# Performance work log

Measured on AMD Instinct MI355X. Metric: run time of the kernel, lower is better.

The kernel has to match this reference:

```python
import jax, jax.numpy as jnp
import numpy as np

B, D = 4096, 2048

def setup_inputs() -> dict:
    key = jax.random.key(0)
    k1, k2 = jax.random.split(key)
    return {
        "cond_feature": jax.random.normal(k1, (B, D), dtype=jnp.float32),
        "sol_feature": jax.random.normal(k2, (B, D), dtype=jnp.float32),
        "temperature": jnp.zeros((), dtype=jnp.float32),
    }

def _l2norm(x):
    # matches torch F.normalize(dim=-1): x / max(||x||, eps)
    n = jnp.linalg.norm(x, axis=-1, keepdims=True)
    return x / jnp.maximum(n, 1e-12)

def reference(cond_feature, sol_feature, temperature):
    c = _l2norm(cond_feature.reshape(cond_feature.shape[0], -1))
    s = _l2norm(sol_feature.reshape(sol_feature.shape[0], -1))
    sim = jnp.einsum('bd,nd->bn', c, s)          # [B, B]
    sim = jnp.maximum(sim, 0.0) * jnp.exp(temperature)
    # cross-entropy with labels = arange(B): mean(logsumexp(row) - diag)
    diag = jnp.diagonal(sim)
    loss_r = jnp.mean(jax.scipy.special.logsumexp(sim, axis=1) - diag)
    loss_c = jnp.mean(jax.scipy.special.logsumexp(sim, axis=0) - diag)
    return (loss_r + loss_c) * 0.5
```

## Files before the change

kernel.cpp:

```cpp
#include <hip/hip_runtime.h>
#include <hip/hip_bf16.h>

#define B_N 4096
#define D_K 2048
#define RB  1024

typedef __attribute__((ext_vector_type(4))) int   i32x4;
typedef __attribute__((ext_vector_type(8))) int   i32x8;
typedef __attribute__((ext_vector_type(4))) float f32x4;

__device__ __forceinline__ i32x8 mk8(i32x4 lo) {
    return (i32x8){lo[0], lo[1], lo[2], lo[3], 0, 0, 0, 0};
}

__device__ __forceinline__ void gl_lds16(const void* g, void* l) {
    __builtin_amdgcn_global_load_lds(
        (const __attribute__((address_space(1))) unsigned int*)g,
        (__attribute__((address_space(3))) unsigned int*)l,
        16, 0, 0);
}

__device__ __forceinline__ unsigned int qe2m1(float v) {
    unsigned int s = (__builtin_bit_cast(unsigned int, v) >> 31) << 3;
    float av = fabsf(v);
    unsigned int c = (av >= 0.25f) + (av >= 0.75f) + (av >= 1.25f) + (av >= 1.75f)
                   + (av >= 2.5f)  + (av >= 3.5f)  + (av >= 5.0f);
    return s | c;
}

__global__ __launch_bounds__(256) void knorm4(const float* __restrict__ C,
                                              const float* __restrict__ S,
                                              unsigned char* __restrict__ Cq,
                                              unsigned char* __restrict__ Sq,
                                              float* __restrict__ rowsum,
                                              float* __restrict__ colsum) {
    int b = blockIdx.x;
    const float* X;
    unsigned char* Y;
    if (b < B_N) { X = C + (size_t)b * D_K; Y = Cq + (size_t)b * RB; }
    else         { X = S + (size_t)(b - B_N) * D_K; Y = Sq + (size_t)(b - B_N) * RB; }
    int tid = threadIdx.x;

    if (tid == 0) {
        if (b < B_N) rowsum[b] = 0.f;
        else         colsum[b - B_N] = 0.f;
    }

    float4 v0 = ((const float4*)X)[tid * 2];
    float4 v1 = ((const float4*)X)[tid * 2 + 1];
    float ss = v0.x*v0.x + v0.y*v0.y + v0.z*v0.z + v0.w*v0.w
             + v1.x*v1.x + v1.y*v1.y + v1.z*v1.z + v1.w*v1.w;
    #pragma unroll
    for (int off = 1; off < 64; off <<= 1) ss += __shfl_xor(ss, off, 64);
    __shared__ float wsum[4];
    if ((tid & 63) == 0) wsum[tid >> 6] = ss;
    __syncthreads();
    float tot = wsum[0] + wsum[1] + wsum[2] + wsum[3];
    float inv = 64.f / fmaxf(sqrtf(tot), 1e-12f);

    float vals[8] = { v0.x, v0.y, v0.z, v0.w, v1.x, v1.y, v1.z, v1.w };
    unsigned int u = 0;
    #pragma unroll
    for (int j = 0; j < 8; ++j)
        u |= qe2m1(vals[j] * inv) << (4 * j);
    *(unsigned int*)(Y + tid * 4) = u;
}


#define SBK 256
#define NST (D_K / SBK)

__global__ __launch_bounds__(256, 2) void kgemm_q4(const unsigned char* __restrict__ Aq,
                                                   const unsigned char* __restrict__ Bq,
                                                   const float* __restrict__ temp,
                                                   float* __restrict__ rowsum,
                                                   float* __restrict__ colsum,
                                                   float* __restrict__ diag) {
    __shared__ __align__(16) unsigned char As[128 * 128];
    __shared__ __align__(16) unsigned char Bs[256 * 128];

    const int tid  = threadIdx.x;
    const int lane = tid & 63;
    const int wn   = tid >> 6;
    const int brow = blockIdx.x * 128;
    const int bcol = blockIdx.y * 256;

    const int srow = tid >> 3;
    const int sch  = ((tid & 7) ^ (srow & 7)) * 16;
    const unsigned char* gA = Aq + (size_t)(brow + srow) * RB + sch;
    const unsigned char* gB = Bq + (size_t)(bcol + srow) * RB + sch;

    const int lrow = lane & 15;
    const int kq   = lane >> 4;
    const int sw   = lrow & 7;
    const int ch0  = ((kq)     ^ sw) * 16;
    const int ch1  = ((4 + kq) ^ sw) * 16;
    const int abase = lrow * 128;
    const int bbase = (wn * 64 + lrow) * 128;

    f32x4 acc[8][4];
    #pragma unroll
    for (int m = 0; m < 8; ++m)
        #pragma unroll
        for (int n = 0; n < 4; ++n) acc[m][n] = (f32x4){0.f, 0.f, 0.f, 0.f};

    for (int st = 0; st < NST; ++st) {
        const int k0b = st * 128;
        #pragma unroll
        for (int i = 0; i < 4; ++i)
            gl_lds16(gA + k0b + (size_t)(32 * i) * RB, As + tid * 16 + i * 4096);
        #pragma unroll
        for (int i = 0; i < 8; ++i)
            gl_lds16(gB + k0b + (size_t)(32 * i) * RB, Bs + tid * 16 + i * 4096);
        __syncthreads();

        #pragma unroll
        for (int h = 0; h < 2; ++h) {
            const int ch = h ? ch1 : ch0;
            i32x4 b0 = *(const i32x4*)(Bs + bbase + 0 * 2048 + ch);
            i32x4 b1 = *(const i32x4*)(Bs + bbase + 1 * 2048 + ch);
            i32x4 b2 = *(const i32x4*)(Bs + bbase + 2 * 2048 + ch);
            i32x4 b3 = *(const i32x4*)(Bs + bbase + 3 * 2048 + ch);
            __builtin_amdgcn_sched_barrier(0);

            #define QMMA(mm) do { \
                i32x4 a_ = *(const i32x4*)(As + abase + (mm) * 2048 + ch); \
                i32x8 a8 = mk8(a_); \
                acc[mm][0] = __builtin_amdgcn_mfma_scale_f32_16x16x128_f8f6f4( \
                    a8, mk8(b0), acc[mm][0], 4, 4, 0, 127, 0, 127); \
                acc[mm][1] = __builtin_amdgcn_mfma_scale_f32_16x16x128_f8f6f4( \
                    a8, mk8(b1), acc[mm][1], 4, 4, 0, 127, 0, 127); \
                acc[mm][2] = __builtin_amdgcn_mfma_scale_f32_16x16x128_f8f6f4( \
                    a8, mk8(b2), acc[mm][2], 4, 4, 0, 127, 0, 127); \
                acc[mm][3] = __builtin_amdgcn_mfma_scale_f32_16x16x128_f8f6f4( \
                    a8, mk8(b3), acc[mm][3], 4, 4, 0, 127, 0, 127); \
                __builtin_amdgcn_sched_barrier(0); \
            } while (0)

            QMMA(0); QMMA(1); QMMA(2); QMMA(3);
            QMMA(4); QMMA(5); QMMA(6); QMMA(7);
            #undef QMMA
        }
        __syncthreads();
    }

    const float scl = expf(temp[0]);
    const int cbase = bcol + wn * 64 + lrow;
    const int rj = kq * 4;

    float cs[4] = {0.f, 0.f, 0.f, 0.f};
    #pragma unroll
    for (int m = 0; m < 8; ++m) {
        float rs[4] = {0.f, 0.f, 0.f, 0.f};
        #pragma unroll
        for (int n = 0; n < 4; ++n) {
            #pragma unroll
            for (int j = 0; j < 4; ++j) {
                float sim = acc[m][n][j] * (1.f / 4096.f);
                float v = fmaxf(sim, 0.f) * scl;
                int gr = brow + m * 16 + rj + j;
                int gc = cbase + n * 16;
                if (gr == gc) diag[gr] = v;
                float p = expf(v - scl);
                rs[j]  += p;
                cs[n]  += p;
            }
        }
        #pragma unroll
        for (int j = 0; j < 4; ++j) {
            float v = rs[j];
            v += __shfl_xor(v, 1, 64);
            v += __shfl_xor(v, 2, 64);
            v += __shfl_xor(v, 4, 64);
            v += __shfl_xor(v, 8, 64);
            if (lrow == 0) atomicAdd(&rowsum[brow + m * 16 + rj + j], v);
        }
    }
    #pragma unroll
    for (int n = 0; n < 4; ++n) {
        float v = cs[n];
        v += __shfl_xor(v, 16, 64);
        v += __shfl_xor(v, 32, 64);
        if (kq == 0) atomicAdd(&colsum[cbase + n * 16], v);
    }
}

__global__ __launch_bounds__(256) void kfinal(const float* __restrict__ rowsum,
                                              const float* __restrict__ colsum,
                                              const float* __restrict__ diag,
                                              const float* __restrict__ temp,
                                              float* __restrict__ out) {
    int tid = threadIdx.x;
    float M = expf(temp[0]);
    float acc = 0.f;
    for (int i = tid; i < B_N; i += 256) {
        acc += logf(rowsum[i]) + logf(colsum[i]) + 2.f * M - 2.f * diag[i];
    }
    #pragma unroll
    for (int off = 1; off < 64; off <<= 1) acc += __shfl_xor(acc, off, 64);
    __shared__ float wsum[4];
    if ((tid & 63) == 0) wsum[tid >> 6] = acc;
    __syncthreads();
    if (tid == 0) {
        float t = wsum[0] + wsum[1] + wsum[2] + wsum[3];
        out[0] = t * (0.5f / (float)B_N);
    }
}

extern "C" void kernel_launch(void* const* d_in, const int* in_sizes, int n_in,
                              void* d_out, int out_size, void* d_ws, size_t ws_size,
                              hipStream_t stream) {
    const float* Cf   = (const float*)d_in[0];
    const float* Sf   = (const float*)d_in[1];
    const float* temp = (const float*)d_in[2];

    const size_t MATB = (size_t)B_N * RB;
    unsigned char* Cq = (unsigned char*)d_ws;
    unsigned char* Sq = Cq + MATB;
    float* rowsum = (float*)(Sq + MATB);
    float* colsum = rowsum + B_N;
    float* diag   = colsum + B_N;

    knorm4<<<2 * B_N, 256, 0, stream>>>(Cf, Sf, Cq, Sq, rowsum, colsum);
    dim3 grid(B_N / 128, B_N / 256);
    kgemm_q4<<<grid, 256, 0, stream>>>(Cq, Sq, temp, rowsum, colsum, diag);
    kfinal<<<1, 256, 0, stream>>>(rowsum, colsum, diag, temp, (float*)d_out);
}
```

Before: 54.61 us.

## Shrink GEMM block tile to 128x128 with 2x2 wave grid

Changes the FP4 GEMM block tile from 128x256 to 128x128 and arranges the four waves as a 2x2 grid, each computing a 64x64 sub-tile instead of 128x64. This halves LDS use and accumulator registers per wave, so more blocks can be resident and the grid has twice as many blocks, which helps fill the GPU. In exchange, more A/B data is reloaded across blocks, and more atomics are issued for the row and column sums.

```diff
diff --git a/kernel.cpp b/kernel.cpp
--- a/kernel.cpp
+++ b/kernel.cpp
@@ -77,13 +77,15 @@
                                                    float* __restrict__ colsum,
                                                    float* __restrict__ diag) {
     __shared__ __align__(16) unsigned char As[128 * 128];
-    __shared__ __align__(16) unsigned char Bs[256 * 128];
+    __shared__ __align__(16) unsigned char Bs[128 * 128];
 
     const int tid  = threadIdx.x;
     const int lane = tid & 63;
-    const int wn   = tid >> 6;
+    const int wid  = tid >> 6;
+    const int wr   = wid >> 1;
+    const int wc   = wid & 1;
     const int brow = blockIdx.x * 128;
-    const int bcol = blockIdx.y * 256;
+    const int bcol = blockIdx.y * 128;
 
     const int srow = tid >> 3;
     const int sch  = ((tid & 7) ^ (srow & 7)) * 16;
@@ -95,85 +97,86 @@
     const int sw   = lrow & 7;
     const int ch0  = ((kq)     ^ sw) * 16;
     const int ch1  = ((4 + kq) ^ sw) * 16;
-    const int abase = lrow * 128;
-    const int bbase = (wn * 64 + lrow) * 128;
-
-    f32x4 acc[8][4];
-    #pragma unroll
-    for (int m = 0; m < 8; ++m)
+    const int abase = (wr * 64 + lrow) * 128;
+    const int bbase = (wc * 64 + lrow) * 128;
+
+    f32x4 acc[4][4];
+    #pragma unroll
+    for (int m = 0; m < 4; ++m)
         #pragma unroll
         for (int n = 0; n < 4; ++n) acc[m][n] = (f32x4){0.f, 0.f, 0.f, 0.f};
 
     for (int st = 0; st < NST; ++st) {
         const int k0b = st * 128;
         #pragma unroll
-        for (int i = 0; i < 4; ++i)
+        for (int i = 0; i < 4; ++i) {
             gl_lds16(gA + k0b + (size_t)(32 * i) * RB, As + tid * 16 + i * 4096);
-        #pragma unroll
-        for (int i = 0; i < 8; ++i)
             gl_lds16(gB + k0b + (size_t)(32 * i) * RB, Bs + tid * 16 + i * 4096);
+        }
         __syncthreads();
 
         #pragma unroll
         for (int h = 0; h < 2; ++h) {
             const int ch = h ? ch1 : ch0;
-            i32x4 b0 = *(const i32x4*)(Bs + bbase + 0 * 2048 + ch);
-            i32x4 b1 = *(const i32x4*)(Bs + bbase + 1 * 2048 + ch);
-            i32x4 b2 = *(const i32x4*)(Bs + bbase + 2 * 2048 + ch);
-            i32x4 b3 = *(const i32x4*)(Bs + bbase + 3 * 2048 + ch);
+            i32x4 af[4], bf[4];
+            #pragma unroll
+            for (int m = 0; m < 4; ++m) af[m] = *(const i32x4*)(As + abase + m * 2048 + ch);
+            #pragma unroll
+            for (int n = 0; n < 4; ++n) bf[n] = *(const i32x4*)(Bs + bbase + n * 2048 + ch);
+
+            #pragma unroll
+            for (int m = 0; m < 4; ++m)
+                #pragma unroll
+                for (int n = 0; n < 4; ++n)
+                    acc[m][n] = __builtin_amdgcn_mfma_scale_f32_16x16x128_f8f6f4(
+                        mk8(af[m]), mk8(bf[n]), acc[m][n], 4, 4, 0, 127, 0, 127);
             __builtin_amdgcn_sched_barrier(0);
-
-            #define QMMA(mm) do { \
-                i32x4 a_ = *(const i32x4*)(As + abase + (mm) * 2048 + ch); \
-                i32x8 a8 = mk8(a_); \
-                acc[mm][0] = __builtin_amdgcn_mfma_scale_f32_16x16x128_f8f6f4( \
-                    a8, mk8(b0), acc[mm][0], 4, 4, 0, 127, 0, 127); \
-                acc[mm][1] = __builtin_amdgcn_mfma_scale_f32_16x16x128_f8f6f4( \
-                    a8, mk8(b1), acc[mm][1], 4, 4, 0, 127, 0, 127); \
-                acc[mm][2] = __builtin_amdgcn_mfma_scale_f32_16x16x128_f8f6f4( \
-                    a8, mk8(b2), acc[mm][2], 4, 4, 0, 127, 0, 127); \
-                acc[mm][3] = __builtin_amdgcn_mfma_scale_f32_16x16x128_f8f6f4( \
-                    a8, mk8(b3), acc[mm][3], 4, 4, 0, 127, 0, 127); \
-                __builtin_amdgcn_sched_barrier(0); \
-            } while (0)
-
-            QMMA(0); QMMA(1); QMMA(2); QMMA(3);
-            QMMA(4); QMMA(5); QMMA(6); QMMA(7);
-            #undef QMMA
         }
         __syncthreads();
     }
 
     const float scl = expf(temp[0]);
-    const int cbase = bcol + wn * 64 + lrow;
+    const int rbase = brow + wr * 64;
+    const int cbase = bcol + wc * 64 + lrow;
     const int rj = kq * 4;
 
-    float cs[4] = {0.f, 0.f, 0.f, 0.f};
-    #pragma unroll
-    for (int m = 0; m < 8; ++m) {
-        float rs[4] = {0.f, 0.f, 0.f, 0.f};
+    float rs[4][4];
+    float cs[4];
+    #pragma unroll
+    for (int m = 0; m < 4; ++m)
+        #pragma unroll
+        for (int j = 0; j < 4; ++j) rs[m][j] = 0.f;
+    #pragma unroll
+    for (int n = 0; n < 4; ++n) cs[n] = 0.f;
+
+    #pragma unroll
+    for (int m = 0; m < 4; ++m) {
         #pragma unroll
         for (int n = 0; n < 4; ++n) {
             #pragma unroll
             for (int j = 0; j < 4; ++j) {
                 float sim = acc[m][n][j] * (1.f / 4096.f);
                 float v = fmaxf(sim, 0.f) * scl;
-                int gr = brow + m * 16 + rj + j;
+                int gr = rbase + m * 16 + rj + j;
                 int gc = cbase + n * 16;
                 if (gr == gc) diag[gr] = v;
                 float p = expf(v - scl);
-                rs[j]  += p;
-                cs[n]  += p;
+                rs[m][j] += p;
+                cs[n]    += p;
             }
         }
+    }
+
+    #pragma unroll
+    for (int m = 0; m < 4; ++m) {
         #pragma unroll
         for (int j = 0; j < 4; ++j) {
-            float v = rs[j];
+            float v = rs[m][j];
             v += __shfl_xor(v, 1, 64);
             v += __shfl_xor(v, 2, 64);
             v += __shfl_xor(v, 4, 64);
             v += __shfl_xor(v, 8, 64);
-            if (lrow == 0) atomicAdd(&rowsum[brow + m * 16 + rj + j], v);
+            if (lrow == 0) atomicAdd(&rowsum[rbase + m * 16 + rj + j], v);
         }
     }
     #pragma unroll
@@ -222,7 +225,7 @@
     float* diag   = colsum + B_N;
 
     knorm4<<<2 * B_N, 256, 0, stream>>>(Cf, Sf, Cq, Sq, rowsum, colsum);
-    dim3 grid(B_N / 128, B_N / 256);
+    dim3 grid(B_N / 128, B_N / 128);
     kgemm_q4<<<grid, 256, 0, stream>>>(Cq, Sq, temp, rowsum, colsum, diag);
     kfinal<<<1, 256, 0, stream>>>(rowsum, colsum, diag, temp, (float*)d_out);
 }
```

New measurement: 195.5 us. 258% more time.
